# Kernel tuning notes

Hardware: AMD Instinct MI355X
Metric: run time of the kernel (lower is better)

## Reference

```python
import jax, jax.numpy as jnp
import numpy as np

B, M, H, E = 1, 2048, 16, 128
D = H * E          # 2048, model dim
C = 4 * D          # 8192, FFN dim
F = E
G = D
J = D


def setup_inputs() -> dict:
    key = jax.random.key(0)
    k_in, k_wv, k_wk, k_wq, k_wz, k_ffa, k_ffb = jax.random.split(key, 7)
    scale = 0.01
    return {
        "I_in": jax.random.normal(k_in, (B, M, D), dtype=jnp.float32),
        "WV": jax.random.normal(k_wv, (H, E, D), dtype=jnp.float32) * scale,
        "WK": jax.random.normal(k_wk, (H, E, D), dtype=jnp.float32) * scale,
        "WQ": jax.random.normal(k_wq, (H, E, D), dtype=jnp.float32) * scale,
        "WZ": jax.random.normal(k_wz, (H, F, G), dtype=jnp.float32) * scale,
        "WFFA": jax.random.normal(k_ffa, (G, C), dtype=jnp.float32) * scale,
        "WFFB": jax.random.normal(k_ffb, (C, J), dtype=jnp.float32) * scale,
    }


def reference(I_in, WV, WK, WQ, WZ, WFFA, WFFB):
    # QKV projections: [B,M,D] x [H,E,D] -> [B,M,H,E]
    V = jnp.einsum('bmd,hed->bmhe', I_in, WV)
    K = jnp.einsum('bmd,hed->bmhe', I_in, WK)
    Q = jnp.einsum('bmd,hed->bmhe', I_in, WQ)
    # Attention scores [B,M,P,H]; NOTE: no 1/sqrt(E) scaling in the original.
    QK = jnp.einsum('bmhe,bphe->bmph', Q, K)
    # Softmax over keys (p axis = 2), matching torch.softmax(QK, dim=2)
    QK_softmax = jax.nn.softmax(QK, axis=2)
    # Attention output [B,M,H,E]
    AV = jnp.einsum('bmph,bphe->bmhe', QK_softmax, V)
    # Output projection [B,M,G]
    Z = jnp.einsum('bmhf,hfg->bmg', AV, WZ)
    # FFN (no nonlinearity in the original workload)
    FFA = jnp.einsum('bmg,gc->bmc', Z, WFFA)
    FFB = jnp.einsum('bmc,cj->bmj', FFA, WFFB)
    return FFB
```

## Files before the change

### kernel.cpp

```cpp
#include <hip/hip_runtime.h>
#include <hip/hip_bf16.h>
#include <math.h>


typedef __bf16 bf16_t;
typedef __bf16 bf16x8 __attribute__((ext_vector_type(8)));
typedef float  f32x4  __attribute__((ext_vector_type(4)));

#define AS1 __attribute__((address_space(1)))
#define AS3 __attribute__((address_space(3)))

__device__ __forceinline__ void load16_lds(const bf16_t* g, bf16_t* l) {
    __builtin_amdgcn_global_load_lds((AS1 void*)g, (AS3 void*)l, 16, 0, 0);
}

__device__ __forceinline__ void stageA_half(const bf16_t* __restrict__ Ab, int lda,
                                            int k0, int h, bf16_t* slot,
                                            int w, int lane)
{
    #pragma unroll
    for (int j = 0; j < 2; ++j) {
        const int prw = j * 64 + w * 8;
        const int p   = prw + (lane >> 3);
        const int lr  = (p >> 6) * 128 + h * 64 + (p & 63);
        const int lc  = (lane & 7) ^ (p & 7);
        load16_lds(Ab + (long long)lr * lda + k0 + lc * 8, slot + prw * 64);
    }
}
__device__ __forceinline__ void stageB_half(const bf16_t* __restrict__ Bb, int ldb,
                                            int k0, int h, bf16_t* slot,
                                            int w, int lane)
{
    #pragma unroll
    for (int j = 0; j < 2; ++j) {
        const int prw = j * 64 + w * 8;
        const int p   = prw + (lane >> 3);
        const int lr  = (p >> 5) * 64 + h * 32 + (p & 31);
        const int lc  = (lane & 7) ^ (p & 7);
        load16_lds(Bb + (long long)lr * ldb + k0 + lc * 8, slot + prw * 64);
    }
}

#define LOADAF(SL)                                                             \
  _Pragma("unroll") for (int ks = 0; ks < 2; ++ks)                             \
  _Pragma("unroll") for (int mi = 0; mi < 4; ++mi)                             \
      af[ks][mi] = *(const bf16x8*)&(SL)[(wm * 64 + mi * 16 + c15) * 64 +      \
                      (((ks * 4 + q4) ^ (c15 & 7)) * 8)];

#define LOADBV(DST, SL)                                                        \
  _Pragma("unroll") for (int ks = 0; ks < 2; ++ks)                             \
  _Pragma("unroll") for (int nj = 0; nj < 2; ++nj)                             \
      DST[ks][nj] = *(const bf16x8*)&(SL)[(wn * 32 + nj * 16 + c15) * 64 +     \
                      (((ks * 4 + q4) ^ (c15 & 7)) * 8)];

#define MFMA16(MH, NH, BV)                                                     \
  __builtin_amdgcn_s_setprio(1);                                               \
  _Pragma("unroll") for (int ks = 0; ks < 2; ++ks)                             \
  _Pragma("unroll") for (int mi = 0; mi < 4; ++mi)                             \
  _Pragma("unroll") for (int nj = 0; nj < 2; ++nj)                             \
      acc[(MH) * 4 + mi][(NH) * 2 + nj] =                                      \
          __builtin_amdgcn_mfma_f32_16x16x32_bf16(                             \
              af[ks][mi], BV[ks][nj], acc[(MH) * 4 + mi][(NH) * 2 + nj],       \
              0, 0, 0);                                                        \
  __builtin_amdgcn_s_setprio(0);

#define VMW(N) asm volatile("s_waitcnt vmcnt(" #N ")" ::: "memory")
#define BAR()  __builtin_amdgcn_s_barrier()

template<typename TOUT>
__global__ __launch_bounds__(512, 2)
void gemm256d_bt(const bf16_t* __restrict__ A, const bf16_t* __restrict__ B,
                 TOUT* __restrict__ Cc, int Kdim,
                 int lda, int ldb, int ldc,
                 long long ab, long long bb, long long cb,
                 int ct_z, bf16_t* __restrict__ ctc, int ldct)
{
    __shared__ __attribute__((aligned(16))) bf16_t As[4][128 * 64];
    __shared__ __attribute__((aligned(16))) bf16_t Bs[4][128 * 64];

    const int z = blockIdx.z;
    A  += (long long)z * ab;
    B  += (long long)z * bb;
    Cc += (long long)z * cb;

    const int bm = blockIdx.y * 256;
    const int bn = blockIdx.x * 256;
    const int t = threadIdx.x, lane = t & 63, w = t >> 6;
    const int wm = w >> 2, wn = w & 3;
    const int q4 = lane >> 4, c15 = lane & 15;

    const bf16_t* Ab = A + (long long)bm * lda;
    const bf16_t* Bb = B + (long long)bn * ldb;

    f32x4  acc[8][4] = {};
    bf16x8 af[2][4];
    bf16x8 bv0[2][2];
    bf16x8 bv1[2][2];

    stageA_half(Ab, lda, 0,  0, As[0], w, lane);
    stageB_half(Bb, ldb, 0,  0, Bs[0], w, lane);
    stageB_half(Bb, ldb, 0,  1, Bs[1], w, lane);
    stageA_half(Ab, lda, 0,  1, As[1], w, lane);
    stageA_half(Ab, lda, 64, 0, As[2], w, lane);
    stageB_half(Bb, ldb, 64, 0, Bs[2], w, lane);
    stageB_half(Bb, ldb, 64, 1, Bs[3], w, lane);

    const int NT = Kdim >> 6;

    for (int kt = 0; kt + 2 < NT; ++kt) {
        const int par = kt & 1;
        bf16_t* a0 = As[2 * par];
        bf16_t* a1 = As[2 * par + 1];
        bf16_t* b0 = Bs[2 * par];
        bf16_t* b1 = Bs[2 * par + 1];
        bf16_t* a1n = As[2 * (par ^ 1) + 1];
        const int kn1 = (kt + 1) << 6, kn2 = (kt + 2) << 6;
        VMW(10); BAR();
        stageA_half(Ab, lda, kn1, 1, a1n, w, lane);
        LOADAF(a0); LOADBV(bv0, b0);
        MFMA16(0, 0, bv0);
        VMW(10); BAR();
        LOADBV(bv1, b1);
        MFMA16(0, 1, bv1);
        VMW(8); BAR();
        stageA_half(Ab, lda, kn2, 0, a0, w, lane);
        stageB_half(Bb, ldb, kn2, 0, b0, w, lane);
        LOADAF(a1);
        MFMA16(1, 1, bv1);
        stageB_half(Bb, ldb, kn2, 1, b1, w, lane);
        MFMA16(1, 0, bv0);
    }
    {
        const int kt = NT - 2, par = kt & 1;
        bf16_t* a0 = As[2 * par];
        bf16_t* a1 = As[2 * par + 1];
        bf16_t* b0 = Bs[2 * par];
        bf16_t* b1 = Bs[2 * par + 1];
        bf16_t* a1n = As[2 * (par ^ 1) + 1];
        const int kn1 = (kt + 1) << 6;
        VMW(10); BAR();
        stageA_half(Ab, lda, kn1, 1, a1n, w, lane);
        LOADAF(a0); LOADBV(bv0, b0);
        MFMA16(0, 0, bv0);
        VMW(10); BAR();
        LOADBV(bv1, b1);
        MFMA16(0, 1, bv1);
        VMW(8); BAR();
        LOADAF(a1);
        MFMA16(1, 1, bv1);
        MFMA16(1, 0, bv0);
    }
    {
        const int par = (NT - 1) & 1;
        bf16_t* a0 = As[2 * par];
        bf16_t* a1 = As[2 * par + 1];
        bf16_t* b0 = Bs[2 * par];
        bf16_t* b1 = Bs[2 * par + 1];
        VMW(4); BAR();
        LOADAF(a0); LOADBV(bv0, b0);
        MFMA16(0, 0, bv0);
        VMW(2); BAR();
        LOADBV(bv1, b1);
        MFMA16(0, 1, bv1);
        VMW(0); BAR();
        LOADAF(a1);
        MFMA16(1, 1, bv1);
        MFMA16(1, 0, bv0);
    }

    const int rb = q4 * 4;
    if (z == ct_z) {
        #pragma unroll
        for (int mi = 0; mi < 8; ++mi) {
            const long long mb = bm + wm * 128 + mi * 16 + rb;
            #pragma unroll
            for (int nj = 0; nj < 4; ++nj) {
                const long long n = bn + wn * 64 + nj * 16 + c15;
                union { bf16_t b[4]; unsigned long long u; } o;
                #pragma unroll
                for (int r = 0; r < 4; ++r) o.b[r] = (bf16_t)acc[mi][nj][r];
                *(unsigned long long*)(ctc + n * ldct + mb) = o.u;
            }
        }
    } else {
        #pragma unroll
        for (int mi = 0; mi < 8; ++mi) {
            #pragma unroll
            for (int r = 0; r < 4; ++r) {
                const long long m = bm + wm * 128 + mi * 16 + rb + r;
                TOUT* crow = Cc + m * ldc + bn + wn * 64 + c15;
                #pragma unroll
                for (int nj = 0; nj < 4; ++nj)
                    crow[nj * 16] = (TOUT)acc[mi][nj][r];
            }
        }
    }
}

template<typename TOUT, bool ATOMIC>
__global__ __launch_bounds__(256)
void gemm_bt(const bf16_t* __restrict__ A, const bf16_t* __restrict__ B,
             TOUT* __restrict__ Cc, int Mdim, int Ndim, int Kdim,
             int lda, int ldb, int ldc,
             long long ab, long long bb, long long cb,
             int ct_z, bf16_t* __restrict__ ctc, int ldct)
{
    __shared__ bf16_t Ash[128 * 32];
    __shared__ bf16_t Bsh[128 * 32];

    const int z = blockIdx.z;
    A  += (long long)z * ab;
    B  += (long long)z * bb;
    Cc += (long long)z * cb;

    const int bm = blockIdx.y * 128;
    const int bn = blockIdx.x * 128;
    const int t  = threadIdx.x;
    const int lane = t & 63;
    const int w    = t >> 6;

    const int wm = (w & 1) * 64;
    const int wn = (w >> 1) * 64;

    const int sub = lane >> 2;
    const int seg = lane & 3;

    const bf16_t* Ag0 = A + (long long)(bm + w * 32 + sub) * lda + seg * 8;
    const bf16_t* Ag1 = Ag0 + 16LL * lda;
    const bf16_t* Bg0 = B + (long long)(bn + w * 32 + sub) * ldb + seg * 8;
    const bf16_t* Bg1 = Bg0 + 16LL * ldb;

    bf16_t* Al0 = &Ash[(w * 2 + 0) * 512];
    bf16_t* Al1 = &Ash[(w * 2 + 1) * 512];
    bf16_t* Bl0 = &Bsh[(w * 2 + 0) * 512];
    bf16_t* Bl1 = &Bsh[(w * 2 + 1) * 512];

    const int col  = lane & 15;
    const int koff = (lane >> 4) * 8;

    f32x4 acc[4][4] = {};

    for (int k0 = 0; k0 < Kdim; k0 += 32) {
        load16_lds(Ag0 + k0, Al0);
        load16_lds(Ag1 + k0, Al1);
        load16_lds(Bg0 + k0, Bl0);
        load16_lds(Bg1 + k0, Bl1);
        __syncthreads();

        bf16x8 afr[4], bfr[4];
        #pragma unroll
        for (int mi = 0; mi < 4; ++mi)
            afr[mi] = *(const bf16x8*)&Ash[(wm + mi * 16 + col) * 32 + koff];
        #pragma unroll
        for (int nj = 0; nj < 4; ++nj)
            bfr[nj] = *(const bf16x8*)&Bsh[(wn + nj * 16 + col) * 32 + koff];
        #pragma unroll
        for (int mi = 0; mi < 4; ++mi)
            #pragma unroll
            for (int nj = 0; nj < 4; ++nj)
                acc[mi][nj] = __builtin_amdgcn_mfma_f32_16x16x32_bf16(
                    afr[mi], bfr[nj], acc[mi][nj], 0, 0, 0);
        __syncthreads();
    }

    const int rbase = (lane >> 4) * 4;
    if (z == ct_z) {
        #pragma unroll
        for (int mi = 0; mi < 4; ++mi) {
            const long long mb = bm + wm + mi * 16 + rbase;
            #pragma unroll
            for (int nj = 0; nj < 4; ++nj) {
                const long long n = bn + wn + nj * 16 + col;
                union { bf16_t b[4]; unsigned long long u; } o;
                #pragma unroll
                for (int r = 0; r < 4; ++r) o.b[r] = (bf16_t)acc[mi][nj][r];
                *(unsigned long long*)(ctc + n * ldct + mb) = o.u;
            }
        }
    } else {
        #pragma unroll
        for (int mi = 0; mi < 4; ++mi) {
            #pragma unroll
            for (int r = 0; r < 4; ++r) {
                long long m = bm + wm + mi * 16 + rbase + r;
                TOUT* crow = Cc + m * ldc + bn + wn + col;
                #pragma unroll
                for (int nj = 0; nj < 4; ++nj) {
                    if constexpr (ATOMIC)
                        atomicAdd(&crow[nj * 16], (float)acc[mi][nj][r]);
                    else
                        crow[nj * 16] = (TOUT)acc[mi][nj][r];
                }
            }
        }
    }
}

__global__ __launch_bounds__(256, 2)
void flash_attn(const bf16_t* __restrict__ Q, const bf16_t* __restrict__ K,
                const bf16_t* __restrict__ VT, bf16_t* __restrict__ O,
                int M, int D)
{
    __shared__ bf16_t Kt[64 * 128];
    __shared__ bf16_t Vt[128 * 64];
    __shared__ bf16_t Pl[4 * 16 * 88];

    const int t = threadIdx.x, lane = t & 63, w = t >> 6;
    const int q4 = lane >> 4;
    const int c  = lane & 15;
    const int bm = blockIdx.x * 64;
    const int hE = blockIdx.y * 128;

    bf16x8 af_q[4];
    {
        const bf16_t* qrow = Q + (long long)(bm + w * 16 + c) * D + hE + q4 * 8;
        #pragma unroll
        for (int ks = 0; ks < 4; ++ks)
            af_q[ks] = *(const bf16x8*)(qrow + ks * 32);
    }

    f32x4 acc_o[8] = {};
    float m_i[4] = {-INFINITY, -INFINITY, -INFINITY, -INFINITY};
    float l_i[4] = {0.f, 0.f, 0.f, 0.f};

    bf16_t* Pw = &Pl[w * 16 * 88];

    for (int p0 = 0; p0 < M; p0 += 64) {
        #pragma unroll
        for (int j = 0; j < 4; ++j) {
            int krow = w * 16 + j * 4;
            load16_lds(K + (long long)(p0 + krow + q4) * D + hE + ((c ^ (j * 4 + q4)) * 8),
                       &Kt[krow * 128]);
            int vrow = w * 32 + j * 8;
            load16_lds(VT + (long long)(hE + vrow + (lane >> 3)) * M + p0
                          + (((lane & 7) ^ (lane >> 3)) * 8),
                       &Vt[vrow * 64]);
        }
        __syncthreads();

        f32x4 acc_s[4] = {};
        #pragma unroll
        for (int ks = 0; ks < 4; ++ks) {
            #pragma unroll
            for (int nj = 0; nj < 4; ++nj) {
                int row = nj * 16 + c;
                bf16x8 bk = *(const bf16x8*)&Kt[row * 128 + (((ks * 4 + q4) ^ c) * 8)];
                acc_s[nj] = __builtin_amdgcn_mfma_f32_16x16x32_bf16(
                    af_q[ks], bk, acc_s[nj], 0, 0, 0);
            }
        }

        float mt[4], alpha[4], rs[4];
        #pragma unroll
        for (int r = 0; r < 4; ++r) {
            float v = fmaxf(fmaxf(acc_s[0][r], acc_s[1][r]),
                            fmaxf(acc_s[2][r], acc_s[3][r]));
            #pragma unroll
            for (int off = 1; off < 16; off <<= 1)
                v = fmaxf(v, __shfl_xor(v, off));
            mt[r] = v;
        }
        #pragma unroll
        for (int r = 0; r < 4; ++r) {
            float mn = fmaxf(m_i[r], mt[r]);
            alpha[r] = __expf(m_i[r] - mn);
            m_i[r] = mn;
            rs[r] = 0.f;
        }
        #pragma unroll
        for (int nj = 0; nj < 4; ++nj)
            #pragma unroll
            for (int r = 0; r < 4; ++r) {
                float p = __expf(acc_s[nj][r] - m_i[r]);
                rs[r] += p;
                Pw[(q4 * 4 + r) * 88 + nj * 16 + c] = (bf16_t)p;
            }
        #pragma unroll
        for (int r = 0; r < 4; ++r) {
            float v = rs[r];
            #pragma unroll
            for (int off = 1; off < 16; off <<= 1)
                v += __shfl_xor(v, off);
            l_i[r] = alpha[r] * l_i[r] + v;
        }
        #pragma unroll
        for (int nj = 0; nj < 8; ++nj)
            #pragma unroll
            for (int r = 0; r < 4; ++r)
                acc_o[nj][r] *= alpha[r];
        __syncthreads();

        #pragma unroll
        for (int ks = 0; ks < 2; ++ks) {
            bf16x8 ap = *(const bf16x8*)&Pw[c * 88 + ks * 32 + q4 * 8];
            #pragma unroll
            for (int nj = 0; nj < 8; ++nj) {
                int row = nj * 16 + c;
                bf16x8 bvv = *(const bf16x8*)&Vt[row * 64 + (((ks * 4 + q4) ^ (c & 7)) * 8)];
                acc_o[nj] = __builtin_amdgcn_mfma_f32_16x16x32_bf16(
                    ap, bvv, acc_o[nj], 0, 0, 0);
            }
        }
        __syncthreads();
    }

    float inv[4];
    #pragma unroll
    for (int r = 0; r < 4; ++r) inv[r] = 1.0f / l_i[r];
    #pragma unroll
    for (int nj = 0; nj < 8; ++nj)
        #pragma unroll
        for (int r = 0; r < 4; ++r)
            O[(long long)(bm + w * 16 + q4 * 4 + r) * D + hE + nj * 16 + c] =
                (bf16_t)(acc_o[nj][r] * inv[r]);
}

__global__ __launch_bounds__(256)
void cast4_bf16(const float* __restrict__ s0, const float* __restrict__ s1,
                const float* __restrict__ s2, const float* __restrict__ s3,
                bf16_t* __restrict__ d0, long long seg, long long n)
{
    const float* src = (blockIdx.y == 0) ? s0 : (blockIdx.y == 1) ? s1
                     : (blockIdx.y == 2) ? s2 : s3;
    bf16_t* dst = d0 + (long long)blockIdx.y * seg;
    long long i = ((long long)blockIdx.x * 256 + threadIdx.x) * 4;
    if (i >= n) return;
    float4 v = *(const float4*)(src + i);
    union { bf16_t b[4]; unsigned long long u; } o;
    o.b[0] = (bf16_t)v.x; o.b[1] = (bf16_t)v.y;
    o.b[2] = (bf16_t)v.z; o.b[3] = (bf16_t)v.w;
    *(unsigned long long*)(dst + i) = o.u;
}

__global__ __launch_bounds__(256)
void transpose_to_bf16(const float* __restrict__ in, bf16_t* __restrict__ out,
                       int rows, int cols)
{
    __shared__ bf16_t tile[32][33];
    const int r0 = blockIdx.y * 32, c0 = blockIdx.x * 32;
    const int tx = threadIdx.x & 31, ty = threadIdx.x >> 5;
    #pragma unroll
    for (int i = 0; i < 4; ++i) {
        int r = ty + i * 8;
        tile[r][tx] = (bf16_t)in[(long long)(r0 + r) * cols + c0 + tx];
    }
    __syncthreads();
    #pragma unroll
    for (int i = 0; i < 4; ++i) {
        int r = ty + i * 8;
        out[(long long)(c0 + r) * rows + r0 + tx] = tile[tx][r];
    }
}

__global__ __launch_bounds__(256)
void reduce4_f32(const float* __restrict__ p, float* __restrict__ out,
                 long long n)
{
    long long i = ((long long)blockIdx.x * 256 + threadIdx.x) * 4;
    if (i >= n) return;
    float4 a = *(const float4*)(p + i);
    float4 b = *(const float4*)(p + n + i);
    float4 c = *(const float4*)(p + 2 * n + i);
    float4 d = *(const float4*)(p + 3 * n + i);
    float4 o;
    o.x = a.x + b.x + c.x + d.x;
    o.y = a.y + b.y + c.y + d.y;
    o.z = a.z + b.z + c.z + d.z;
    o.w = a.w + b.w + c.w + d.w;
    *(float4*)(out + i) = o;
}

extern "C" void kernel_launch(void* const* d_in, const int* in_sizes, int n_in,
                              void* d_out, int out_size, void* d_ws, size_t ws_size,
                              hipStream_t stream)
{
    const float* I    = (const float*)d_in[0];
    const float* WV   = (const float*)d_in[1];
    const float* WK   = (const float*)d_in[2];
    const float* WQ   = (const float*)d_in[3];
    const float* WZ   = (const float*)d_in[4];
    const float* WFFA = (const float*)d_in[5];
    const float* WFFB = (const float*)d_in[6];
    float* out = (float*)d_out;

    const int M = 2048, D = 2048, C = 8192;
    const long long MD = (long long)M * D;
    const size_t MiB = 1024 * 1024;

    char* base = (char*)d_ws;
    bf16_t* bI     = (bf16_t*)(base + 0 * MiB);
    bf16_t* bWQ    = (bf16_t*)(base + 8 * MiB);
    bf16_t* bWK    = (bf16_t*)(base + 16 * MiB);
    bf16_t* bWV    = (bf16_t*)(base + 24 * MiB);
    bf16_t* bQ     = (bf16_t*)(base + 32 * MiB);
    bf16_t* bK     = (bf16_t*)(base + 40 * MiB);
    bf16_t* bVT    = (bf16_t*)(base + 48 * MiB);
    bf16_t* bAV    = (bf16_t*)(base + 56 * MiB);
    bf16_t* bZ     = (bf16_t*)(base + 64 * MiB);
    bf16_t* bWZT   = (bf16_t*)(base + 72 * MiB);
    bf16_t* bWFFAT = (bf16_t*)(base + 80 * MiB);
    bf16_t* bWFFBT = (bf16_t*)(base + 112 * MiB);
    bf16_t* bFFA   = (bf16_t*)(base + 0 * MiB);
    float*  pF     = (float*)(base + 32 * MiB);

    const dim3 blk(256);
    const dim3 blk512(512);

    cast4_bf16<<<dim3(MD / 1024, 4), blk, 0, stream>>>(I, WQ, WK, WV, bI, MD, MD);
    transpose_to_bf16<<<dim3(D / 32, D / 32), blk, 0, stream>>>(WZ,   bWZT,   D, D);
    transpose_to_bf16<<<dim3(C / 32, D / 32), blk, 0, stream>>>(WFFA, bWFFAT, D, C);
    transpose_to_bf16<<<dim3(D / 32, C / 32), blk, 0, stream>>>(WFFB, bWFFBT, C, D);

    gemm256d_bt<bf16_t><<<dim3(8, 8, 3), blk512, 0, stream>>>(
        bI, bWQ, bQ, D, D, D, D, 0, MD, MD, 2, bVT, M);

    flash_attn<<<dim3(M / 64, 16), blk, 0, stream>>>(bQ, bK, bVT, bAV, M, D);

    gemm_bt<bf16_t, false><<<dim3(16, 16, 1), blk, 0, stream>>>(
        bAV, bWZT, bZ, M, D, D, D, D, D, 0, 0, 0, -1, nullptr, 0);

    gemm256d_bt<bf16_t><<<dim3(32, 8, 1), blk512, 0, stream>>>(
        bZ, bWFFAT, bFFA, D, D, D, C, 0, 0, 0, -1, nullptr, 0);

    gemm256d_bt<float><<<dim3(8, 8, 4), blk512, 0, stream>>>(
        bFFA, bWFFBT, pF, 2048, C, C, D, 2048, 2048, MD, -1, nullptr, 0);

    reduce4_f32<<<dim3((int)(MD / 1024)), blk, 0, stream>>>(pF, out, MD);
}
```

Before: 631.2 us.

## Software-pipeline LDS fragment reads one phase ahead in the bf16 GEMM main loop

Restructures the GEMM K-loop into four phases per tile, unrolled by two with ping-pong register buffers for the A and B fragments. Each phase's LDS reads are issued ahead of the MFMAs that need them, with explicit lgkmcnt waits and sched_barrier fences, so LDS latency is meant to overlap matrix math. The separate epilogue blocks are replaced by a uniform tail that issues redundant dummy global loads to keep the vmcnt accounting consistent. The trade-offs are more live fragment registers, which raises spill risk at 2 waves per SIMD, and an implicit assumption that the tile count along K is even.

```diff
diff --git a/kernel.cpp b/kernel.cpp
--- a/kernel.cpp
+++ b/kernel.cpp
@@ -41,10 +41,10 @@
     }
 }
 
-#define LOADAF(SL)                                                             \
+#define LOADAF(DST, SL)                                                        \
   _Pragma("unroll") for (int ks = 0; ks < 2; ++ks)                             \
   _Pragma("unroll") for (int mi = 0; mi < 4; ++mi)                             \
-      af[ks][mi] = *(const bf16x8*)&(SL)[(wm * 64 + mi * 16 + c15) * 64 +      \
+      DST[ks][mi] = *(const bf16x8*)&(SL)[(wm * 64 + mi * 16 + c15) * 64 +     \
                       (((ks * 4 + q4) ^ (c15 & 7)) * 8)];
 
 #define LOADBV(DST, SL)                                                        \
@@ -53,19 +53,51 @@
       DST[ks][nj] = *(const bf16x8*)&(SL)[(wn * 32 + nj * 16 + c15) * 64 +     \
                       (((ks * 4 + q4) ^ (c15 & 7)) * 8)];
 
-#define MFMA16(MH, NH, BV)                                                     \
-  __builtin_amdgcn_s_setprio(1);                                               \
+#define MFMA8(R0, C0, AF, BV)                                                  \
   _Pragma("unroll") for (int ks = 0; ks < 2; ++ks)                             \
   _Pragma("unroll") for (int mi = 0; mi < 4; ++mi)                             \
   _Pragma("unroll") for (int nj = 0; nj < 2; ++nj)                             \
-      acc[(MH) * 4 + mi][(NH) * 2 + nj] =                                      \
-          __builtin_amdgcn_mfma_f32_16x16x32_bf16(                             \
-              af[ks][mi], BV[ks][nj], acc[(MH) * 4 + mi][(NH) * 2 + nj],       \
-              0, 0, 0);                                                        \
-  __builtin_amdgcn_s_setprio(0);
-
-#define VMW(N) asm volatile("s_waitcnt vmcnt(" #N ")" ::: "memory")
-#define BAR()  __builtin_amdgcn_s_barrier()
+      acc[(R0) + mi][(C0) + nj] = __builtin_amdgcn_mfma_f32_16x16x32_bf16(     \
+          AF[ks][mi], BV[ks][nj], acc[(R0) + mi][(C0) + nj], 0, 0, 0);
+
+#define VMW(N)  asm volatile("s_waitcnt vmcnt(" #N ")" ::: "memory")
+#define LGKM(N) asm volatile("s_waitcnt lgkmcnt(" #N ")" ::: "memory")
+#define SB()    __builtin_amdgcn_sched_barrier(0)
+#define BAR()   __builtin_amdgcn_s_barrier()
+#define PRIO1   __builtin_amdgcn_s_setprio(1)
+#define PRIO0   __builtin_amdgcn_s_setprio(0)
+
+#define PH0(P, Q, BV0, KA1)                                                    \
+  VMW(8); BAR();                                                               \
+  stageA_half(Ab, lda, (KA1), 1, As[2 * (Q) + 1], w, lane);                    \
+  LOADBV(bv1, Bs[2 * (P) + 1]);                                                \
+  LGKM(4); SB();                                                               \
+  PRIO1; MFMA8(0, 0, af0, BV0); PRIO0;
+
+#define PH1(P)                                                                 \
+  VMW(8); BAR();                                                               \
+  LOADAF(af1, As[2 * (P) + 1]);                                                \
+  LGKM(8); SB();                                                               \
+  PRIO1; MFMA8(0, 2, af0, bv1); PRIO0;
+
+#define PH2(P, KN2)                                                            \
+  stageA_half(Ab, lda, (KN2), 0, As[2 * (P)], w, lane);                        \
+  stageB_half(Bb, ldb, (KN2), 0, Bs[2 * (P)], w, lane);                        \
+  LGKM(0); SB();                                                               \
+  PRIO1; MFMA8(4, 2, af1, bv1); PRIO0;
+
+#define PH3(P, Q, BV0, BV0N, KN2, DOREAD)                                      \
+  VMW(8); BAR();                                                               \
+  stageB_half(Bb, ldb, (KN2), 1, Bs[2 * (P) + 1], w, lane);                    \
+  if constexpr (DOREAD) { LOADAF(af0, As[2 * (Q)]); LOADBV(BV0N, Bs[2 * (Q)]); } \
+  SB();                                                                        \
+  PRIO1; MFMA8(4, 0, af1, BV0); PRIO0;
+
+#define KTILE(P, Q, BV0, BV0N, KA1, KN2, DOREAD)                               \
+  PH0(P, Q, BV0, KA1)                                                          \
+  PH1(P)                                                                       \
+  PH2(P, KN2)                                                                  \
+  PH3(P, Q, BV0, BV0N, KN2, DOREAD)
 
 template<typename TOUT>
 __global__ __launch_bounds__(512, 2)
@@ -93,9 +125,9 @@
     const bf16_t* Bb = B + (long long)bn * ldb;
 
     f32x4  acc[8][4] = {};
-    bf16x8 af[2][4];
-    bf16x8 bv0[2][2];
+    bf16x8 af0[2][4], af1[2][4];
     bf16x8 bv1[2][2];
+    bf16x8 bv0e[2][2], bv0o[2][2];
 
     stageA_half(Ab, lda, 0,  0, As[0], w, lane);
     stageB_half(Bb, ldb, 0,  0, Bs[0], w, lane);
@@ -104,68 +136,23 @@
     stageA_half(Ab, lda, 64, 0, As[2], w, lane);
     stageB_half(Bb, ldb, 64, 0, Bs[2], w, lane);
     stageB_half(Bb, ldb, 64, 1, Bs[3], w, lane);
+    VMW(10); BAR();
+    LOADAF(af0, As[0]);
+    LOADBV(bv0e, Bs[0]);
 
     const int NT = Kdim >> 6;
 
-    for (int kt = 0; kt + 2 < NT; ++kt) {
-        const int par = kt & 1;
-        bf16_t* a0 = As[2 * par];
-        bf16_t* a1 = As[2 * par + 1];
-        bf16_t* b0 = Bs[2 * par];
-        bf16_t* b1 = Bs[2 * par + 1];
-        bf16_t* a1n = As[2 * (par ^ 1) + 1];
-        const int kn1 = (kt + 1) << 6, kn2 = (kt + 2) << 6;
-        VMW(10); BAR();
-        stageA_half(Ab, lda, kn1, 1, a1n, w, lane);
-        LOADAF(a0); LOADBV(bv0, b0);
-        MFMA16(0, 0, bv0);
-        VMW(10); BAR();
-        LOADBV(bv1, b1);
-        MFMA16(0, 1, bv1);
-        VMW(8); BAR();
-        stageA_half(Ab, lda, kn2, 0, a0, w, lane);
-        stageB_half(Bb, ldb, kn2, 0, b0, w, lane);
-        LOADAF(a1);
-        MFMA16(1, 1, bv1);
-        stageB_half(Bb, ldb, kn2, 1, b1, w, lane);
-        MFMA16(1, 0, bv0);
+    for (int kt = 0; kt + 3 < NT; kt += 2) {
+        const int kA1e = (kt + 1) << 6;
+        const int kN2e = (kt + 2) << 6;
+        const int kN2o = (kt + 3) << 6;
+        KTILE(0, 1, bv0e, bv0o, kA1e, kN2e, 1)
+        KTILE(1, 0, bv0o, bv0e, kN2e, kN2o, 1)
     }
     {
-        const int kt = NT - 2, par = kt & 1;
-        bf16_t* a0 = As[2 * par];
-        bf16_t* a1 = As[2 * par + 1];
-        bf16_t* b0 = Bs[2 * par];
-        bf16_t* b1 = Bs[2 * par + 1];
-        bf16_t* a1n = As[2 * (par ^ 1) + 1];
-        const int kn1 = (kt + 1) << 6;
-        VMW(10); BAR();
-        stageA_half(Ab, lda, kn1, 1, a1n, w, lane);
-        LOADAF(a0); LOADBV(bv0, b0);
-        MFMA16(0, 0, bv0);
-        VMW(10); BAR();
-        LOADBV(bv1, b1);
-        MFMA16(0, 1, bv1);
-        VMW(8); BAR();
-        LOADAF(a1);
-        MFMA16(1, 1, bv1);
-        MFMA16(1, 0, bv0);
-    }
-    {
-        const int par = (NT - 1) & 1;
-        bf16_t* a0 = As[2 * par];
-        bf16_t* a1 = As[2 * par + 1];
-        bf16_t* b0 = Bs[2 * par];
-        bf16_t* b1 = Bs[2 * par + 1];
-        VMW(4); BAR();
-        LOADAF(a0); LOADBV(bv0, b0);
-        MFMA16(0, 0, bv0);
-        VMW(2); BAR();
-        LOADBV(bv1, b1);
-        MFMA16(0, 1, bv1);
-        VMW(0); BAR();
-        LOADAF(a1);
-        MFMA16(1, 1, bv1);
-        MFMA16(1, 0, bv0);
+        const int KD = (NT - 1) << 6;
+        KTILE(0, 1, bv0e, bv0o, KD, KD, 1)
+        KTILE(1, 0, bv0o, bv0e, KD, KD, 0)
     }
 
     const int rb = q4 * 4;
```

New measurement: 908.4 us. 43.9% more time.
